# Optimization experiments

Measured on AMD Instinct MI355X. Metric: run time of the kernel, lower is better.

## Reference

```python
import jax, jax.numpy as jnp
import numpy as np

B, F, K, VOCAB = 16384, 39, 64, 1000000
HID = [10, 5, 3]


def setup_inputs() -> dict:
    key = jax.random.key(0)
    ks = jax.random.split(key, 12)
    feature = jax.random.randint(ks[0], (B, F), 0, VOCAB)
    v_table = jax.random.normal(ks[1], (VOCAB, K), dtype=jnp.float32) * 0.01
    w_table = jax.random.normal(ks[2], (VOCAB, 1), dtype=jnp.float32) * 0.01
    w0 = jnp.zeros((1,), dtype=jnp.float32)
    d_in = F * K
    def lin(kw, kb, din, dout):
        s = 1.0 / np.sqrt(din)
        W = jax.random.uniform(kw, (din, dout), minval=-s, maxval=s, dtype=jnp.float32)
        b = jax.random.uniform(kb, (dout,), minval=-s, maxval=s, dtype=jnp.float32)
        return W, b
    W0, b0 = lin(ks[3], ks[4], d_in, HID[0])
    W1, b1 = lin(ks[5], ks[6], HID[0], HID[1])
    W2, b2 = lin(ks[7], ks[8], HID[1], HID[2])
    W3, b3 = lin(ks[9], ks[10], HID[2], 1)
    return {"feature": feature, "v_table": v_table, "w_table": w_table, "w0": w0,
            "W0": W0, "b0": b0, "W1": W1, "b1": b1, "W2": W2, "b2": b2, "W3": W3, "b3": b3}


def reference(feature, v_table, w_table, w0, W0, b0, W1, b1, W2, b2, W3, b3):
    # Embedding gather: [B, F, K]
    V = v_table[feature]
    # FM pairwise term sum_{i<j} V_i . V_j = 0.5*(||sum_i V_i||^2 - sum_i ||V_i||^2)
    s = jnp.sum(V, axis=1)                       # [B, K]
    fm = 0.5 * (jnp.sum(s * s, axis=-1) - jnp.sum(V * V, axis=(1, 2)))  # [B]
    # Linear (first-order) term
    lin = jnp.sum(w_table[feature], axis=(1, 2))  # [B]
    # Tiny DNN on flattened embeddings
    h = V.reshape(V.shape[0], -1)                 # [B, F*K]
    h = jax.nn.relu(h @ W0 + b0)
    h = jax.nn.relu(h @ W1 + b1)
    h = jax.nn.relu(h @ W2 + b2)
    dnn = h @ W3 + b3                             # [B, 1]
    return fm[:, None] + lin[:, None] + w0 + dnn  # [B, 1]
```

## Files before the change

### kernel.cpp

```cpp
#include <hip/hip_runtime.h>
#include <hip/hip_bf16.h>

#define NF 39
#define NK 64
#define NROW (NF * NK)

__device__ __forceinline__ float bf_lo(unsigned u) { return __uint_as_float(u << 16); }
__device__ __forceinline__ float bf_hi(unsigned u) { return __uint_as_float(u & 0xffff0000u); }

__device__ __forceinline__ unsigned f2bf(float f) {
    unsigned u = __float_as_uint(f);
    return (u + 0x7fffu + ((u >> 16) & 1u)) >> 16;
}

__global__ __launch_bounds__(512, 2)
void deepfm_kernel(const int* __restrict__ feature,
                   const float* __restrict__ v_table,
                   const float* __restrict__ w_table,
                   const float* __restrict__ w0s,
                   const float* __restrict__ W0,
                   const float* __restrict__ b0,
                   const float* __restrict__ W1,
                   const float* __restrict__ b1,
                   const float* __restrict__ W2,
                   const float* __restrict__ b2,
                   const float* __restrict__ W3,
                   const float* __restrict__ b3,
                   float* __restrict__ out)
{
    __shared__ unsigned w0_lds[5 * NROW];

    for (int i = threadIdx.x; i < NROW; i += 512) {
        #pragma unroll
        for (int jp = 0; jp < 5; ++jp) {
            unsigned lo = f2bf(W0[i * 10 + 2 * jp]);
            unsigned hi = f2bf(W0[i * 10 + 2 * jp + 1]);
            w0_lds[jp * NROW + i] = lo | (hi << 16);
        }
    }
    __syncthreads();

    const int lane = threadIdx.x & 63;
    const int wave = threadIdx.x >> 6;
    const int s0   = blockIdx.x * 32 + wave * 4;

    float h0p[4][10];
    float sv[4], sq[4], lin[4];
    #pragma unroll
    for (int s = 0; s < 4; ++s) {
        sv[s] = 0.f; sq[s] = 0.f; lin[s] = 0.f;
        #pragma unroll
        for (int j = 0; j < 10; ++j) h0p[s][j] = 0.f;
    }

    #pragma unroll 2
    for (int f = 0; f < NF; ++f) {
        int   idx[4];
        float v[4];
        #pragma unroll
        for (int s = 0; s < 4; ++s) {
            idx[s] = feature[(s0 + s) * NF + f];
            v[s]   = v_table[(size_t)idx[s] * NK + lane];
            lin[s] += w_table[idx[s]];
        }
        unsigned u[5];
        #pragma unroll
        for (int jp = 0; jp < 5; ++jp)
            u[jp] = w0_lds[jp * NROW + f * NK + lane];
        #pragma unroll
        for (int s = 0; s < 4; ++s) {
            sv[s] += v[s];
            sq[s]  = fmaf(v[s], v[s], sq[s]);
            #pragma unroll
            for (int jp = 0; jp < 5; ++jp) {
                h0p[s][2 * jp]     = fmaf(v[s], bf_lo(u[jp]), h0p[s][2 * jp]);
                h0p[s][2 * jp + 1] = fmaf(v[s], bf_hi(u[jp]), h0p[s][2 * jp + 1]);
            }
        }
    }

    const float w0v = w0s[0];

    #pragma unroll
    for (int s = 0; s < 4; ++s) {
        float t = fmaf(sv[s], sv[s], -sq[s]);
        #pragma unroll
        for (int m = 1; m < 64; m <<= 1) {
            t += __shfl_xor(t, m, 64);
            #pragma unroll
            for (int j = 0; j < 10; ++j)
                h0p[s][j] += __shfl_xor(h0p[s][j], m, 64);
        }
        float h0v[10];
        #pragma unroll
        for (int j = 0; j < 10; ++j) h0v[j] = fmaxf(h0p[s][j] + b0[j], 0.f);
        float h1[5];
        #pragma unroll
        for (int p = 0; p < 5; ++p) {
            float a = b1[p];
            #pragma unroll
            for (int j = 0; j < 10; ++j) a = fmaf(h0v[j], W1[j * 5 + p], a);
            h1[p] = fmaxf(a, 0.f);
        }
        float h2[3];
        #pragma unroll
        for (int q = 0; q < 3; ++q) {
            float a = b2[q];
            #pragma unroll
            for (int p = 0; p < 5; ++p) a = fmaf(h1[p], W2[p * 3 + q], a);
            h2[q] = fmaxf(a, 0.f);
        }
        float dnn = b3[0];
        #pragma unroll
        for (int q = 0; q < 3; ++q) dnn = fmaf(h2[q], W3[q], dnn);

        if (lane == 0) out[s0 + s] = 0.5f * t + lin[s] + w0v + dnn;
    }
}

extern "C" void kernel_launch(void* const* d_in, const int* in_sizes, int n_in,
                              void* d_out, int out_size, void* d_ws, size_t ws_size,
                              hipStream_t stream) {
    const int*   feature = (const int*)  d_in[0];
    const float* v_table = (const float*)d_in[1];
    const float* w_table = (const float*)d_in[2];
    const float* w0s     = (const float*)d_in[3];
    const float* W0      = (const float*)d_in[4];
    const float* b0      = (const float*)d_in[5];
    const float* W1      = (const float*)d_in[6];
    const float* b1      = (const float*)d_in[7];
    const float* W2      = (const float*)d_in[8];
    const float* b2      = (const float*)d_in[9];
    const float* W3      = (const float*)d_in[10];
    const float* b3      = (const float*)d_in[11];

    deepfm_kernel<<<dim3(512), dim3(512), 0, stream>>>(
        feature, v_table, w_table, w0s, W0, b0, W1, b1, W2, b2, W3, b3,
        (float*)d_out);
}
```

Baseline: 52.51 us.

## Remap wave lanes to 4 samples x 16 lanes with float4 embedding loads

Each wave's 64 lanes now split into 4 groups of 16. Each group handles one sample, and each lane loads a float4 (4 consecutive k values) of the embedding row. The per-sample DNN epilogue now runs once per lane-group, and the reduction shrinks to 4 shuffle steps instead of 4 samples x 6 steps, which cuts shuffle and epilogue work. This also replaces scalar loads with vectorized global and LDS (uint4) loads. In exchange, each lane issues one gather per feature, and the h0 accumulators are reduced in registers before the shuffle.

After: 44.46 us (median of 2 runs). 15.3% less time.

```diff
diff --git a/kernel.cpp b/kernel.cpp
--- a/kernel.cpp
+++ b/kernel.cpp
@@ -43,79 +43,86 @@
     const int lane = threadIdx.x & 63;
     const int wave = threadIdx.x >> 6;
     const int s0   = blockIdx.x * 32 + wave * 4;
+    const int sg   = lane >> 4;
+    const int kq   = lane & 15;
+
+    const int* fptr = feature + (size_t)(s0 + sg) * NF;
 
     float h0p[4][10];
-    float sv[4], sq[4], lin[4];
+    float sv[4], sq[4];
+    float lin = 0.f;
     #pragma unroll
-    for (int s = 0; s < 4; ++s) {
-        sv[s] = 0.f; sq[s] = 0.f; lin[s] = 0.f;
+    for (int i = 0; i < 4; ++i) {
+        sv[i] = 0.f; sq[i] = 0.f;
         #pragma unroll
-        for (int j = 0; j < 10; ++j) h0p[s][j] = 0.f;
+        for (int j = 0; j < 10; ++j) h0p[i][j] = 0.f;
     }
 
     #pragma unroll 2
     for (int f = 0; f < NF; ++f) {
-        int   idx[4];
-        float v[4];
+        const int idx = fptr[f];
+        lin += w_table[idx];
+        const float4 v4 = ((const float4*)(v_table + ((size_t)(unsigned)idx << 6)))[kq];
+        const float vv[4] = { v4.x, v4.y, v4.z, v4.w };
         #pragma unroll
-        for (int s = 0; s < 4; ++s) {
-            idx[s] = feature[(s0 + s) * NF + f];
-            v[s]   = v_table[(size_t)idx[s] * NK + lane];
-            lin[s] += w_table[idx[s]];
+        for (int i = 0; i < 4; ++i) {
+            sv[i] += vv[i];
+            sq[i]  = fmaf(vv[i], vv[i], sq[i]);
         }
-        unsigned u[5];
         #pragma unroll
-        for (int jp = 0; jp < 5; ++jp)
-            u[jp] = w0_lds[jp * NROW + f * NK + lane];
-        #pragma unroll
-        for (int s = 0; s < 4; ++s) {
-            sv[s] += v[s];
-            sq[s]  = fmaf(v[s], v[s], sq[s]);
-            #pragma unroll
-            for (int jp = 0; jp < 5; ++jp) {
-                h0p[s][2 * jp]     = fmaf(v[s], bf_lo(u[jp]), h0p[s][2 * jp]);
-                h0p[s][2 * jp + 1] = fmaf(v[s], bf_hi(u[jp]), h0p[s][2 * jp + 1]);
-            }
+        for (int jp = 0; jp < 5; ++jp) {
+            const uint4 u = *(const uint4*)&w0_lds[jp * NROW + f * NK + kq * 4];
+            h0p[0][2*jp]   = fmaf(vv[0], bf_lo(u.x), h0p[0][2*jp]);
+            h0p[0][2*jp+1] = fmaf(vv[0], bf_hi(u.x), h0p[0][2*jp+1]);
+            h0p[1][2*jp]   = fmaf(vv[1], bf_lo(u.y), h0p[1][2*jp]);
+            h0p[1][2*jp+1] = fmaf(vv[1], bf_hi(u.y), h0p[1][2*jp+1]);
+            h0p[2][2*jp]   = fmaf(vv[2], bf_lo(u.z), h0p[2][2*jp]);
+            h0p[2][2*jp+1] = fmaf(vv[2], bf_hi(u.z), h0p[2][2*jp+1]);
+            h0p[3][2*jp]   = fmaf(vv[3], bf_lo(u.w), h0p[3][2*jp]);
+            h0p[3][2*jp+1] = fmaf(vv[3], bf_hi(u.w), h0p[3][2*jp+1]);
         }
     }
 
+    float t = 0.f;
+    #pragma unroll
+    for (int i = 0; i < 4; ++i) t += fmaf(sv[i], sv[i], -sq[i]);
+    float hj[10];
+    #pragma unroll
+    for (int j = 0; j < 10; ++j)
+        hj[j] = (h0p[0][j] + h0p[1][j]) + (h0p[2][j] + h0p[3][j]);
+    #pragma unroll
+    for (int m = 1; m < 16; m <<= 1) {
+        t += __shfl_xor(t, m, 64);
+        #pragma unroll
+        for (int j = 0; j < 10; ++j)
+            hj[j] += __shfl_xor(hj[j], m, 64);
+    }
+
     const float w0v = w0s[0];
+    float h0v[10];
+    #pragma unroll
+    for (int j = 0; j < 10; ++j) h0v[j] = fmaxf(hj[j] + b0[j], 0.f);
+    float h1[5];
+    #pragma unroll
+    for (int p = 0; p < 5; ++p) {
+        float a = b1[p];
+        #pragma unroll
+        for (int j = 0; j < 10; ++j) a = fmaf(h0v[j], W1[j * 5 + p], a);
+        h1[p] = fmaxf(a, 0.f);
+    }
+    float h2[3];
+    #pragma unroll
+    for (int q = 0; q < 3; ++q) {
+        float a = b2[q];
+        #pragma unroll
+        for (int p = 0; p < 5; ++p) a = fmaf(h1[p], W2[p * 3 + q], a);
+        h2[q] = fmaxf(a, 0.f);
+    }
+    float dnn = b3[0];
+    #pragma unroll
+    for (int q = 0; q < 3; ++q) dnn = fmaf(h2[q], W3[q], dnn);
 
-    #pragma unroll
-    for (int s = 0; s < 4; ++s) {
-        float t = fmaf(sv[s], sv[s], -sq[s]);
-        #pragma unroll
-        for (int m = 1; m < 64; m <<= 1) {
-            t += __shfl_xor(t, m, 64);
-            #pragma unroll
-            for (int j = 0; j < 10; ++j)
-                h0p[s][j] += __shfl_xor(h0p[s][j], m, 64);
-        }
-        float h0v[10];
-        #pragma unroll
-        for (int j = 0; j < 10; ++j) h0v[j] = fmaxf(h0p[s][j] + b0[j], 0.f);
-        float h1[5];
-        #pragma unroll
-        for (int p = 0; p < 5; ++p) {
-            float a = b1[p];
-            #pragma unroll
-            for (int j = 0; j < 10; ++j) a = fmaf(h0v[j], W1[j * 5 + p], a);
-            h1[p] = fmaxf(a, 0.f);
-        }
-        float h2[3];
-        #pragma unroll
-        for (int q = 0; q < 3; ++q) {
-            float a = b2[q];
-            #pragma unroll
-            for (int p = 0; p < 5; ++p) a = fmaf(h1[p], W2[p * 3 + q], a);
-            h2[q] = fmaxf(a, 0.f);
-        }
-        float dnn = b3[0];
-        #pragma unroll
-        for (int q = 0; q < 3; ++q) dnn = fmaf(h2[q], W3[q], dnn);
-
-        if (lane == 0) out[s0 + s] = 0.5f * t + lin[s] + w0v + dnn;
-    }
+    if (kq == 0) out[s0 + sg] = 0.5f * t + lin + w0v + dnn;
 }
 
 extern "C" void kernel_launch(void* const* d_in, const int* in_sizes, int n_in,
```
